# Kernel tuning notes

Hardware: AMD Instinct MI355X
Metric: run time of the kernel (lower is better)

Reference implementation:

```python
import jax, jax.numpy as jnp
import numpy as np

VOCAB, D = 50000, 300
B, LC = 64, 32
T, LT = 256, 64
N_SENTS = 5


def setup_inputs() -> dict:
    key = jax.random.key(0)
    k1, k2, k3 = jax.random.split(key, 3)
    claim = jax.random.randint(k1, (B, LC), 0, VOCAB)
    targets = jax.random.randint(k2, (B, T, LT), 0, VOCAB)
    embeddings = jax.random.normal(k3, (VOCAB, D), dtype=jnp.float32)
    return {"claim": claim, "targets": targets, "embeddings": embeddings, "n": N_SENTS}


def reference(claim, targets, embeddings, n):
    # Embedding lookups (frozen table)
    c = embeddings[claim]          # [B, Lc, d]
    t = embeddings[targets]        # [B, T, Lt, d]
    # batch_U = claim[:,None] @ targets^T  -> [B, T, Lc, Lt]
    U = jnp.einsum('bcd,btld->btcl', c, t)
    # softmax over target tokens (axis=3), max over claim tokens (axis=2)
    sm = jax.nn.softmax(U, axis=3)
    scores = jnp.max(sm, axis=2)           # [B, T, Lt]
    target_scores = jnp.sum(scores, axis=2)  # [B, T]
    # per-batch top-n target sentences (sorted order; torch used sorted=False,
    # the selected set is identical)
    _, idx = jax.lax.top_k(target_scores, n)  # [B, n]
    top = jnp.take_along_axis(U, idx[:, :, None, None], axis=1)  # [B, n, Lc, Lt]
    # L2-normalize over last axis (torch dim=2 of the [n, Lc, Lt] slice)
    norm = jnp.sqrt(jnp.sum(top * top, axis=3, keepdims=True))
    return top / norm
```

## Files before the change

### kernel.cpp

```cpp
#include <hip/hip_runtime.h>

#define VOCAB 50000
#define D     300
#define B_    64
#define LC    32
#define T_    256
#define LT    64
#define NSEL  5
#define NCAND 16

#define A_U4   2560
#define A_HALF 20480
#define TROW   320

typedef _Float16 half8_t __attribute__((ext_vector_type(8)));
typedef float    f32x4   __attribute__((ext_vector_type(4)));


__global__ __launch_bounds__(256) void k_prep(const int* __restrict__ claim,
                                              const float* __restrict__ emb,
                                              _Float16* __restrict__ tab,
                                              _Float16* __restrict__ wsA,
                                              int tableBlocks) {
    int wave = threadIdx.x >> 6, lane = threadIdx.x & 63;
    if ((int)blockIdx.x < tableBlocks) {
        int r = blockIdx.x * 4 + wave;
        const float* src = emb + (size_t)r * D;
        _Float16* d = tab + (size_t)r * TROW;
#pragma unroll
        for (int i = 0; i < 5; ++i) {
            int k = lane + i * 64;
            d[k] = (k < D) ? (_Float16)src[k] : (_Float16)0.0f;
        }
    } else {
        int row = (blockIdx.x - tableBlocks) * 4 + wave;
        int b = row >> 5, m = row & 31;
        int tok = claim[row];
        const float* src = emb + (size_t)tok * D;
        _Float16* base = wsA + (size_t)b * A_HALF;
#pragma unroll
        for (int i = 0; i < 5; ++i) {
            int k = lane + i * 64;
            float x = (k < D) ? src[k] : 0.0f;
            _Float16 h = (_Float16)x;
            int sp = ((k >> 3) ^ (m & 7));
            int idx = (m * 40 + sp) * 8 + (k & 7);
            base[idx] = h;
            base[10240 + idx] = (_Float16)(x - (float)h);
        }
    }
}

__device__ __forceinline__ void split8(const float4& a, const float4& b,
                                       half8_t& hv, half8_t& lv) {
    float x[8] = {a.x, a.y, a.z, a.w, b.x, b.y, b.z, b.w};
#pragma unroll
    for (int i = 0; i < 8; ++i) {
        _Float16 h = (_Float16)x[i];
        hv[i] = h;
        lv[i] = (_Float16)(x[i] - (float)h);
    }
}

template<int NI>
__device__ __forceinline__ void compute_exact(const uint4* sA,
                                              const float* __restrict__ emb,
                                              const int* __restrict__ trow, int lcol0,
                                              int lane, f32x4 acc[2][NI]) {
    int ln = lane & 15, quad = lane >> 4;
#pragma unroll
    for (int mi = 0; mi < 2; ++mi)
#pragma unroll
        for (int ni = 0; ni < NI; ++ni) acc[mi][ni] = (f32x4)0.0f;

    int arow0 = ln * 40;
    int arow1 = (16 + ln) * 40;
    int key = ln & 7;
    int qo = quad * 8;

    const float* bp[NI];
#pragma unroll
    for (int ni = 0; ni < NI; ++ni) {
        int tok = trow[lcol0 + ni * 16 + ln];
        bp[ni] = emb + (size_t)tok * D;
    }
#pragma unroll 1
    for (int ks = 0; ks < 10; ++ks) {
        int kb = ks * 32 + qo;
        int ka = kb > 296 ? 296 : kb;
        int kb4 = kb + 4;
        int kbb = kb4 > 296 ? 296 : kb4;
        float4 b0[NI], b1[NI];
#pragma unroll
        for (int ni = 0; ni < NI; ++ni) {
            b0[ni] = *(const float4*)(bp[ni] + ka);
            b1[ni] = *(const float4*)(bp[ni] + kbb);
        }
        if (kb >= 296) {
            float4 z = make_float4(0.f, 0.f, 0.f, 0.f);
#pragma unroll
            for (int ni = 0; ni < NI; ++ni) {
                if (kb >= 300) b0[ni] = z;
                b1[ni] = z;
            }
        }
        int sp = (ks * 4 + quad) ^ key;
        half8_t ah[2], al[2];
        ah[0] = __builtin_bit_cast(half8_t, sA[arow0 + sp]);
        al[0] = __builtin_bit_cast(half8_t, sA[1280 + arow0 + sp]);
        ah[1] = __builtin_bit_cast(half8_t, sA[arow1 + sp]);
        al[1] = __builtin_bit_cast(half8_t, sA[1280 + arow1 + sp]);
        half8_t bh[NI], bl[NI];
#pragma unroll
        for (int ni = 0; ni < NI; ++ni) split8(b0[ni], b1[ni], bh[ni], bl[ni]);
#pragma unroll
        for (int mi = 0; mi < 2; ++mi)
#pragma unroll
            for (int ni = 0; ni < NI; ++ni) {
                acc[mi][ni] = __builtin_amdgcn_mfma_f32_16x16x32_f16(ah[mi], bh[ni], acc[mi][ni], 0, 0, 0);
                acc[mi][ni] = __builtin_amdgcn_mfma_f32_16x16x32_f16(ah[mi], bl[ni], acc[mi][ni], 0, 0, 0);
                acc[mi][ni] = __builtin_amdgcn_mfma_f32_16x16x32_f16(al[mi], bh[ni], acc[mi][ni], 0, 0, 0);
            }
    }
}

__device__ __forceinline__ void compute_noisy(const uint4* sA,
                                              const _Float16* __restrict__ tab,
                                              const int* __restrict__ trow,
                                              int lane, f32x4 acc[2][4]) {
    int ln = lane & 15, quad = lane >> 4;
#pragma unroll
    for (int mi = 0; mi < 2; ++mi)
#pragma unroll
        for (int ni = 0; ni < 4; ++ni) acc[mi][ni] = (f32x4)0.0f;

    int arow0 = ln * 40;
    int arow1 = (16 + ln) * 40;
    int key = ln & 7;
    int qo = quad * 8;

    const _Float16* rp[4];
#pragma unroll
    for (int ni = 0; ni < 4; ++ni) {
        int tok = trow[ni * 16 + ln];
        rp[ni] = tab + (size_t)tok * TROW;
    }
    half8_t bh[2][4];
#pragma unroll
    for (int ni = 0; ni < 4; ++ni) bh[0][ni] = *(const half8_t*)(rp[ni] + qo);
#pragma unroll
    for (int ks = 0; ks < 10; ++ks) {
        int cur = ks & 1, nxt = cur ^ 1;
        if (ks < 9) {
            int ko = (ks + 1) * 32 + qo;
#pragma unroll
            for (int ni = 0; ni < 4; ++ni)
                bh[nxt][ni] = *(const half8_t*)(rp[ni] + ko);
        }
        int sp = (ks * 4 + quad) ^ key;
        half8_t ah[2], al[2];
        ah[0] = __builtin_bit_cast(half8_t, sA[arow0 + sp]);
        al[0] = __builtin_bit_cast(half8_t, sA[1280 + arow0 + sp]);
        ah[1] = __builtin_bit_cast(half8_t, sA[arow1 + sp]);
        al[1] = __builtin_bit_cast(half8_t, sA[1280 + arow1 + sp]);
#pragma unroll
        for (int mi = 0; mi < 2; ++mi)
#pragma unroll
            for (int ni = 0; ni < 4; ++ni) {
                acc[mi][ni] = __builtin_amdgcn_mfma_f32_16x16x32_f16(ah[mi], bh[cur][ni], acc[mi][ni], 0, 0, 0);
                acc[mi][ni] = __builtin_amdgcn_mfma_f32_16x16x32_f16(al[mi], bh[cur][ni], acc[mi][ni], 0, 0, 0);
            }
    }
}

__device__ __forceinline__ float xmax4(float v) {
    v = fmaxf(v, __shfl_xor(v, 1)); v = fmaxf(v, __shfl_xor(v, 2));
    v = fmaxf(v, __shfl_xor(v, 4)); v = fmaxf(v, __shfl_xor(v, 8));
    return v;
}
__device__ __forceinline__ float xsum4(float v) {
    v += __shfl_xor(v, 1); v += __shfl_xor(v, 2);
    v += __shfl_xor(v, 4); v += __shfl_xor(v, 8);
    return v;
}

__device__ __forceinline__ float score_from_acc(f32x4 acc[2][4]) {
    float score_l[4] = {0.f, 0.f, 0.f, 0.f};
#pragma unroll
    for (int mi = 0; mi < 2; ++mi)
#pragma unroll
        for (int r = 0; r < 4; ++r) {
            float m = fmaxf(fmaxf(acc[mi][0][r], acc[mi][1][r]),
                            fmaxf(acc[mi][2][r], acc[mi][3][r]));
            m = xmax4(m);
            float p[4], s = 0.f;
#pragma unroll
            for (int ni = 0; ni < 4; ++ni) { p[ni] = __expf(acc[mi][ni][r] - m); s += p[ni]; }
            s = xsum4(s);
            float rv = 1.0f / s;
#pragma unroll
            for (int ni = 0; ni < 4; ++ni) score_l[ni] = fmaxf(score_l[ni], p[ni] * rv);
        }
    float tot = 0.f;
#pragma unroll
    for (int ni = 0; ni < 4; ++ni) {
        float v = score_l[ni];
        v = fmaxf(v, __shfl_xor(v, 16));
        v = fmaxf(v, __shfl_xor(v, 32));
        tot += v;
    }
    return xsum4(tot);
}

template<bool FAST>
__global__ __launch_bounds__(256, 4) void k_scores(const int* __restrict__ targets,
                                                   const float* __restrict__ emb,
                                                   const _Float16* __restrict__ tab,
                                                   const _Float16* __restrict__ wsA,
                                                   float* __restrict__ wsScr) {
    __shared__ __align__(16) uint4 sA[A_U4];
    int wg = blockIdx.x;
    int xcd = wg & 7, rest = wg >> 3;
    int b = xcd * 8 + (rest >> 6);
    int tg = rest & 63;
    int tid = threadIdx.x;
    {
        const uint4* src = (const uint4*)(wsA + (size_t)b * A_HALF);
        for (int i = tid; i < A_U4; i += 256) sA[i] = src[i];
    }
    __syncthreads();

    int lane = tid & 63, wave = tid >> 6;
    int t = tg * 4 + wave;
    const int* trow = targets + ((size_t)b * T_ + t) * LT;

    f32x4 acc[2][4];
    if (FAST) compute_noisy(sA, tab, trow, lane, acc);
    else      compute_exact<4>(sA, emb, trow, 0, lane, acc);
    float tot = score_from_acc(acc);
    if (lane == 0) wsScr[b * T_ + t] = tot;
}

__global__ __launch_bounds__(256) void k_sel(const int* __restrict__ targets,
                                             const float* __restrict__ emb,
                                             const _Float16* __restrict__ wsA,
                                             const float* __restrict__ wsScr,
                                             int* __restrict__ wsCand,
                                             float* __restrict__ wsScoreC) {
    __shared__ __align__(16) uint4 sA[A_U4];
    __shared__ int sCand[NCAND];
    int r = blockIdx.x, b = blockIdx.y, tid = threadIdx.x;
    int lane = tid & 63, wave = tid >> 6;
    if (wave) {
        const uint4* src = (const uint4*)(wsA + (size_t)b * A_HALF);
        for (int i = tid - 64; i < A_U4; i += 192) sA[i] = src[i];
    } else {
        float v[4];
#pragma unroll
        for (int i = 0; i < 4; ++i) v[i] = wsScr[b * T_ + lane + 64 * i];
        for (int s = 0; s < NCAND; ++s) {
            float bv = v[0]; int bi = lane;
#pragma unroll
            for (int i = 1; i < 4; ++i) {
                int idx = lane + 64 * i;
                if (v[i] > bv) { bv = v[i]; bi = idx; }
            }
            for (int off = 32; off > 0; off >>= 1) {
                float ov = __shfl_down(bv, off);
                int   oi = __shfl_down(bi, off);
                if (ov > bv || (ov == bv && oi < bi)) { bv = ov; bi = oi; }
            }
            bi = __shfl(bi, 0);
            if (lane == 0) {
                sCand[s] = bi;
                if (r == 0) wsCand[b * NCAND + s] = bi;
            }
            if ((bi & 63) == lane) v[bi >> 6] = -1e30f;
        }
    }
    __syncthreads();

    int c = r * 4 + wave;
    int t = sCand[c];
    const int* trow = targets + ((size_t)b * T_ + t) * LT;
    f32x4 acc[2][4];
    compute_exact<4>(sA, emb, trow, 0, lane, acc);
    float tot = score_from_acc(acc);
    if (lane == 0) wsScoreC[b * NCAND + c] = tot;
}

__global__ __launch_bounds__(256) void k_output(const int* __restrict__ targets,
                                                const float* __restrict__ emb,
                                                const _Float16* __restrict__ wsA,
                                                const int* __restrict__ wsCand,
                                                const float* __restrict__ wsScoreC,
                                                float* __restrict__ out) {
    __shared__ __align__(16) uint4 sA[A_U4];
    __shared__ float sS[LC][4];
    __shared__ int sT;
    int b = blockIdx.y, j = blockIdx.x, tid = threadIdx.x;
    int lane = tid & 63, wave = tid >> 6;
    if (wave) {
        const uint4* src = (const uint4*)(wsA + (size_t)b * A_HALF);
        for (int i = tid - 64; i < A_U4; i += 192) sA[i] = src[i];
    } else if (lane == 0) {
        unsigned used = 0; int sel = 0;
        for (int jj = 0; jj <= j; ++jj) {
            float bs = -1e30f; int bt = 0x7fffffff, bsl = 0;
            for (int s = 0; s < NCAND; ++s) {
                if (used & (1u << s)) continue;
                float sc = wsScoreC[b * NCAND + s];
                int tt = wsCand[b * NCAND + s];
                if (sc > bs || (sc == bs && tt < bt)) { bs = sc; bt = tt; bsl = s; }
            }
            used |= (1u << bsl);
            sel = bt;
        }
        sT = sel;
    }
    __syncthreads();

    int t = sT;
    const int* trow = targets + ((size_t)b * T_ + t) * LT;
    f32x4 acc[2][1];
    compute_exact<1>(sA, emb, trow, wave * 16, lane, acc);

    int ln = lane & 15, quad = lane >> 4;
#pragma unroll
    for (int mi = 0; mi < 2; ++mi)
#pragma unroll
        for (int r = 0; r < 4; ++r) {
            float v = acc[mi][0][r] * acc[mi][0][r];
            v = xsum4(v);
            if (ln == 0) sS[mi * 16 + quad * 4 + r][wave] = v;
        }
    __syncthreads();

    float* obase = out + (size_t)(b * NSEL + j) * (LC * LT);
#pragma unroll
    for (int mi = 0; mi < 2; ++mi)
#pragma unroll
        for (int r = 0; r < 4; ++r) {
            int c = mi * 16 + quad * 4 + r;
            float ss = sS[c][0] + sS[c][1] + sS[c][2] + sS[c][3];
            float rinv = 1.0f / sqrtf(ss);
            obase[c * LT + wave * 16 + ln] = acc[mi][0][r] * rinv;
        }
}

extern "C" void kernel_launch(void* const* d_in, const int* in_sizes, int n_in,
                              void* d_out, int out_size, void* d_ws, size_t ws_size,
                              hipStream_t stream) {
    const int*   claim   = (const int*)d_in[0];
    const int*   targets = (const int*)d_in[1];
    const float* emb     = (const float*)d_in[2];

    const size_t tabBytes = (size_t)VOCAB * TROW * sizeof(_Float16);
    const size_t restBytes = (size_t)B_ * A_HALF * sizeof(_Float16)
                           + (size_t)B_ * T_ * sizeof(float)
                           + (size_t)B_ * NCAND * (sizeof(int) + sizeof(float)) + 256;
    bool fast = ws_size >= tabBytes + restBytes;

    char* p = (char*)d_ws;
    _Float16* tab = nullptr;
    if (fast) { tab = (_Float16*)p; p += tabBytes; }
    _Float16* wsA = (_Float16*)p; p += (size_t)B_ * A_HALF * sizeof(_Float16);
    float* wsScr = (float*)p;     p += (size_t)B_ * T_ * sizeof(float);
    int*   wsCand = (int*)p;      p += (size_t)B_ * NCAND * sizeof(int);
    float* wsScoreC = (float*)p;
    float* out   = (float*)d_out;

    int tableBlocks = fast ? (VOCAB / 4) : 0;
    k_prep<<<dim3(tableBlocks + 512), dim3(256), 0, stream>>>(claim, emb, tab, wsA, tableBlocks);
    if (fast) {
        k_scores<true><<<dim3(B_ * 64), dim3(256), 0, stream>>>(targets, emb, tab, wsA, wsScr);
    } else {
        k_scores<false><<<dim3(B_ * 64), dim3(256), 0, stream>>>(targets, emb, tab, wsA, wsScr);
    }
    k_sel<<<dim3(NCAND / 4, B_), dim3(256), 0, stream>>>(targets, emb, wsA, wsScr, wsCand, wsScoreC);
    k_output<<<dim3(NSEL, B_), dim3(256), 0, stream>>>(targets, emb, wsA, wsCand, wsScoreC, out);
}
```

Baseline: 235.2 us.

## Fuse candidate selection and output into scores kernel via last-block atomic counter

```diff
diff --git a/kernel.cpp b/kernel.cpp
--- a/kernel.cpp
+++ b/kernel.cpp
@@ -21,8 +21,10 @@
                                               const float* __restrict__ emb,
                                               _Float16* __restrict__ tab,
                                               _Float16* __restrict__ wsA,
+                                              int* __restrict__ wsCnt,
                                               int tableBlocks) {
     int wave = threadIdx.x >> 6, lane = threadIdx.x & 63;
+    if ((int)blockIdx.x == tableBlocks && threadIdx.x < B_) wsCnt[threadIdx.x] = 0;
     if ((int)blockIdx.x < tableBlocks) {
         int r = blockIdx.x * 4 + wave;
         const float* src = emb + (size_t)r * D;
@@ -217,7 +219,12 @@
                                                    const float* __restrict__ emb,
                                                    const _Float16* __restrict__ tab,
                                                    const _Float16* __restrict__ wsA,
-                                                   float* __restrict__ wsScr) {
+                                                   float* __restrict__ wsScr,
+                                                   int* __restrict__ wsCand,
+                                                   float* __restrict__ wsScoreC,
+                                                   int* __restrict__ wsCnt,
+                                                   int* __restrict__ wsFlag,
+                                                   float* __restrict__ out) {
     __shared__ __align__(16) uint4 sA[A_U4];
     int wg = blockIdx.x;
     int xcd = wg & 7, rest = wg >> 3;
@@ -234,30 +241,29 @@
     int t = tg * 4 + wave;
     const int* trow = targets + ((size_t)b * T_ + t) * LT;
 
-    f32x4 acc[2][4];
-    if (FAST) compute_noisy(sA, tab, trow, lane, acc);
-    else      compute_exact<4>(sA, emb, trow, 0, lane, acc);
-    float tot = score_from_acc(acc);
-    if (lane == 0) wsScr[b * T_ + t] = tot;
-}
-
-__global__ __launch_bounds__(256) void k_sel(const int* __restrict__ targets,
-                                             const float* __restrict__ emb,
-                                             const _Float16* __restrict__ wsA,
-                                             const float* __restrict__ wsScr,
-                                             int* __restrict__ wsCand,
-                                             float* __restrict__ wsScoreC) {
-    __shared__ __align__(16) uint4 sA[A_U4];
-    __shared__ int sCand[NCAND];
-    int r = blockIdx.x, b = blockIdx.y, tid = threadIdx.x;
-    int lane = tid & 63, wave = tid >> 6;
-    if (wave) {
-        const uint4* src = (const uint4*)(wsA + (size_t)b * A_HALF);
-        for (int i = tid - 64; i < A_U4; i += 192) sA[i] = src[i];
-    } else {
+    {
+        f32x4 acc[2][4];
+        if (FAST) compute_noisy(sA, tab, trow, lane, acc);
+        else      compute_exact<4>(sA, emb, trow, 0, lane, acc);
+        float tot = score_from_acc(acc);
+        if (lane == 0) wsScr[b * T_ + t] = tot;
+    }
+
+    __syncthreads();
+    if (tid == 0) {
+        __threadfence();
+        int prev = atomicAdd(&wsCnt[b], 1);
+        wsFlag[wg] = (prev == B_ - 1);
+    }
+    __syncthreads();
+    if (!wsFlag[wg]) return;
+    __threadfence();
+
+    if (wave == 0) {
         float v[4];
 #pragma unroll
         for (int i = 0; i < 4; ++i) v[i] = wsScr[b * T_ + lane + 64 * i];
+#pragma unroll
         for (int s = 0; s < NCAND; ++s) {
             float bv = v[0]; int bi = lane;
 #pragma unroll
@@ -271,39 +277,26 @@
                 if (ov > bv || (ov == bv && oi < bi)) { bv = ov; bi = oi; }
             }
             bi = __shfl(bi, 0);
-            if (lane == 0) {
-                sCand[s] = bi;
-                if (r == 0) wsCand[b * NCAND + s] = bi;
-            }
+            if (lane == 0) wsCand[b * NCAND + s] = bi;
             if ((bi & 63) == lane) v[bi >> 6] = -1e30f;
         }
     }
     __syncthreads();
 
-    int c = r * 4 + wave;
-    int t = sCand[c];
-    const int* trow = targets + ((size_t)b * T_ + t) * LT;
-    f32x4 acc[2][4];
-    compute_exact<4>(sA, emb, trow, 0, lane, acc);
-    float tot = score_from_acc(acc);
-    if (lane == 0) wsScoreC[b * NCAND + c] = tot;
-}
-
-__global__ __launch_bounds__(256) void k_output(const int* __restrict__ targets,
-                                                const float* __restrict__ emb,
-                                                const _Float16* __restrict__ wsA,
-                                                const int* __restrict__ wsCand,
-                                                const float* __restrict__ wsScoreC,
-                                                float* __restrict__ out) {
-    __shared__ __align__(16) uint4 sA[A_U4];
-    __shared__ float sS[LC][4];
-    __shared__ int sT;
-    int b = blockIdx.y, j = blockIdx.x, tid = threadIdx.x;
-    int lane = tid & 63, wave = tid >> 6;
-    if (wave) {
-        const uint4* src = (const uint4*)(wsA + (size_t)b * A_HALF);
-        for (int i = tid - 64; i < A_U4; i += 192) sA[i] = src[i];
-    } else if (lane == 0) {
+#pragma unroll 1
+    for (int p = 0; p < 4; ++p) {
+        int tc = wsCand[b * NCAND + p * 4 + wave];
+        const int* tr = targets + ((size_t)b * T_ + tc) * LT;
+        f32x4 a2[2][4];
+        compute_exact<4>(sA, emb, tr, 0, lane, a2);
+        float sc = score_from_acc(a2);
+        if (lane == 0) wsScoreC[b * NCAND + p * 4 + wave] = sc;
+    }
+    __syncthreads();
+
+    int ln = lane & 15, quad = lane >> 4;
+#pragma unroll 1
+    for (int j = wave; j < NSEL; j += 4) {
         unsigned used = 0; int sel = 0;
         for (int jj = 0; jj <= j; ++jj) {
             float bs = -1e30f; int bt = 0x7fffffff, bsl = 0;
@@ -316,36 +309,25 @@
             used |= (1u << bsl);
             sel = bt;
         }
-        sT = sel;
-    }
-    __syncthreads();
-
-    int t = sT;
-    const int* trow = targets + ((size_t)b * T_ + t) * LT;
-    f32x4 acc[2][1];
-    compute_exact<1>(sA, emb, trow, wave * 16, lane, acc);
-
-    int ln = lane & 15, quad = lane >> 4;
-#pragma unroll
-    for (int mi = 0; mi < 2; ++mi)
-#pragma unroll
-        for (int r = 0; r < 4; ++r) {
-            float v = acc[mi][0][r] * acc[mi][0][r];
-            v = xsum4(v);
-            if (ln == 0) sS[mi * 16 + quad * 4 + r][wave] = v;
-        }
-    __syncthreads();
-
-    float* obase = out + (size_t)(b * NSEL + j) * (LC * LT);
-#pragma unroll
-    for (int mi = 0; mi < 2; ++mi)
-#pragma unroll
-        for (int r = 0; r < 4; ++r) {
-            int c = mi * 16 + quad * 4 + r;
-            float ss = sS[c][0] + sS[c][1] + sS[c][2] + sS[c][3];
-            float rinv = 1.0f / sqrtf(ss);
-            obase[c * LT + wave * 16 + ln] = acc[mi][0][r] * rinv;
-        }
+        const int* tr = targets + ((size_t)b * T_ + sel) * LT;
+        f32x4 a2[2][4];
+        compute_exact<4>(sA, emb, tr, 0, lane, a2);
+        float* obase = out + (size_t)(b * NSEL + j) * (LC * LT);
+#pragma unroll
+        for (int mi = 0; mi < 2; ++mi)
+#pragma unroll
+            for (int r = 0; r < 4; ++r) {
+                float ssum = 0.f;
+#pragma unroll
+                for (int ni = 0; ni < 4; ++ni) ssum += a2[mi][ni][r] * a2[mi][ni][r];
+                ssum = xsum4(ssum);
+                float rinv = 1.0f / sqrtf(ssum);
+                int c = mi * 16 + quad * 4 + r;
+#pragma unroll
+                for (int ni = 0; ni < 4; ++ni)
+                    obase[c * LT + ni * 16 + ln] = a2[mi][ni][r] * rinv;
+            }
+    }
 }
 
 extern "C" void kernel_launch(void* const* d_in, const int* in_sizes, int n_in,
@@ -358,25 +340,28 @@
     const size_t tabBytes = (size_t)VOCAB * TROW * sizeof(_Float16);
     const size_t restBytes = (size_t)B_ * A_HALF * sizeof(_Float16)
                            + (size_t)B_ * T_ * sizeof(float)
-                           + (size_t)B_ * NCAND * (sizeof(int) + sizeof(float)) + 256;
+                           + (size_t)B_ * NCAND * (sizeof(int) + sizeof(float))
+                           + B_ * sizeof(int) + 4096 * sizeof(int) + 256;
     bool fast = ws_size >= tabBytes + restBytes;
 
     char* p = (char*)d_ws;
     _Float16* tab = nullptr;
     if (fast) { tab = (_Float16*)p; p += tabBytes; }
-    _Float16* wsA = (_Float16*)p; p += (size_t)B_ * A_HALF * sizeof(_Float16);
-    float* wsScr = (float*)p;     p += (size_t)B_ * T_ * sizeof(float);
-    int*   wsCand = (int*)p;      p += (size_t)B_ * NCAND * sizeof(int);
-    float* wsScoreC = (float*)p;
+    _Float16* wsA = (_Float16*)p;  p += (size_t)B_ * A_HALF * sizeof(_Float16);
+    float* wsScr = (float*)p;      p += (size_t)B_ * T_ * sizeof(float);
+    int*   wsCand = (int*)p;       p += (size_t)B_ * NCAND * sizeof(int);
+    float* wsScoreC = (float*)p;   p += (size_t)B_ * NCAND * sizeof(float);
+    int*   wsCnt = (int*)p;        p += B_ * sizeof(int);
+    int*   wsFlag = (int*)p;
     float* out   = (float*)d_out;
 
     int tableBlocks = fast ? (VOCAB / 4) : 0;
-    k_prep<<<dim3(tableBlocks + 512), dim3(256), 0, stream>>>(claim, emb, tab, wsA, tableBlocks);
+    k_prep<<<dim3(tableBlocks + 512), dim3(256), 0, stream>>>(claim, emb, tab, wsA, wsCnt, tableBlocks);
     if (fast) {
-        k_scores<true><<<dim3(B_ * 64), dim3(256), 0, stream>>>(targets, emb, tab, wsA, wsScr);
+        k_scores<true><<<dim3(B_ * 64), dim3(256), 0, stream>>>(
+            targets, emb, tab, wsA, wsScr, wsCand, wsScoreC, wsCnt, wsFlag, out);
     } else {
-        k_scores<false><<<dim3(B_ * 64), dim3(256), 0, stream>>>(targets, emb, tab, wsA, wsScr);
-    }
-    k_sel<<<dim3(NCAND / 4, B_), dim3(256), 0, stream>>>(targets, emb, wsA, wsScr, wsCand, wsScoreC);
-    k_output<<<dim3(NSEL, B_), dim3(256), 0, stream>>>(targets, emb, wsA, wsCand, wsScoreC, out);
-}
+        k_scores<false><<<dim3(B_ * 64), dim3(256), 0, stream>>>(
+            targets, emb, tab, wsA, wsScr, wsCand, wsScoreC, wsCnt, wsFlag, out);
+    }
+}
```

Measured after the change: 488.7 us. 108% more time.
